# Performance work log

Hardware: AMD Instinct MI355X
Metric: run time of the kernel (lower is better)

Reference implementation:

```python
import jax, jax.numpy as jnp
import numpy as np

EMBED, HEADS, FF, WIN = 512, 8, 2048, 64
SIGMA, PSTRENGTH, PERIOD, THRESH = 2.0, 1.0, 100.0, 0.0


def layer_norm(x, g, b, eps=1e-5):
    mu = jnp.mean(x, axis=-1, keepdims=True)
    var = jnp.var(x, axis=-1, keepdims=True)
    return (x - mu) * jax.lax.rsqrt(var + eps) * g + b


def setup_inputs() -> dict:
    key = jax.random.key(0)
    ks = jax.random.split(key, 16)
    s = 1.0 / np.sqrt(EMBED)
    sf = 1.0 / np.sqrt(FF)
    inp = {
        "src": jax.random.normal(ks[0], (8, 2048, EMBED), dtype=jnp.float32),
        "Wq": jax.random.normal(ks[1], (EMBED, EMBED), dtype=jnp.float32) * s,
        "bq": jnp.zeros((EMBED,), jnp.float32),
        "Wk": jax.random.normal(ks[2], (EMBED, EMBED), dtype=jnp.float32) * s,
        "bk": jnp.zeros((EMBED,), jnp.float32),
        "Wv": jax.random.normal(ks[3], (EMBED, EMBED), dtype=jnp.float32) * s,
        "bv": jnp.zeros((EMBED,), jnp.float32),
        "Wo": jax.random.normal(ks[4], (EMBED, EMBED), dtype=jnp.float32) * s,
        "bo": jnp.zeros((EMBED,), jnp.float32),
        "Wg": jax.random.normal(ks[5], (EMBED, 1), dtype=jnp.float32) * s,
        "bg": jnp.zeros((1,), jnp.float32),
        "W1": jax.random.normal(ks[6], (EMBED, FF), dtype=jnp.float32) * s,
        "b1": jnp.zeros((FF,), jnp.float32),
        "W2": jax.random.normal(ks[7], (FF, EMBED), dtype=jnp.float32) * sf,
        "b2": jnp.zeros((EMBED,), jnp.float32),
        "ln1_g": jnp.ones((EMBED,), jnp.float32),
        "ln1_b": jnp.zeros((EMBED,), jnp.float32),
        "ln2_g": jnp.ones((EMBED,), jnp.float32),
        "ln2_b": jnp.zeros((EMBED,), jnp.float32),
    }
    return inp


def gated_sparse_attn(x, Wq, bq, Wk, bk, Wv, bv, Wo, bo, Wg, bg):
    B, S, D = x.shape
    H, dh = HEADS, D // HEADS
    q = (x @ Wq + bq).reshape(B, S, H, dh).transpose(0, 2, 1, 3)  # [B,H,S,dh]
    k = (x @ Wk + bk).reshape(B, S, H, dh).transpose(0, 2, 1, 3)
    v = (x @ Wv + bv).reshape(B, S, H, dh).transpose(0, 2, 1, 3)
    scores = jnp.einsum('bhqd,bhkd->bhqk', q, k) / jnp.sqrt(jnp.float32(dh))
    idx = jnp.arange(S, dtype=jnp.float32)
    dist = idx[:, None] - idx[None, :]  # [S,S]
    gauss_bias = jnp.exp(-(dist * dist) / (2.0 * SIGMA * SIGMA))
    per_bias = PSTRENGTH * jnp.cos(2.0 * jnp.pi * dist / PERIOD)
    scores = scores + gauss_bias + per_bias  # positional biases baked into scores
    local = jnp.abs(dist) <= WIN  # local-window sparsity mask
    scores = jnp.where(local, scores, jnp.float32(-1e9))
    attn = jax.nn.softmax(scores, axis=-1)
    out = jnp.einsum('bhqk,bhkd->bhqd', attn, v)
    out = out.transpose(0, 2, 1, 3).reshape(B, S, D) @ Wo + bo
    gate = jax.nn.sigmoid(x @ Wg + bg)  # [B,S,1] learned gating
    gate = jnp.where(gate > THRESH, gate, jnp.float32(0.0))
    return gate * out


def reference(src, Wq, bq, Wk, bk, Wv, bv, Wo, bo, Wg, bg, W1, b1, W2, b2, ln1_g, ln1_b, ln2_g, ln2_b):
    # dropout is identity in eval mode
    attn_out = gated_sparse_attn(src, Wq, bq, Wk, bk, Wv, bv, Wo, bo, Wg, bg)
    x = layer_norm(src + attn_out, ln1_g, ln1_b)
    ff = jax.nn.relu(x @ W1 + b1) @ W2 + b2
    return layer_norm(x + ff, ln2_g, ln2_b)
```

## Files before the change

kernel.cpp:

```cpp
#include <hip/hip_runtime.h>
#include <hip/hip_bf16.h>
#include <math.h>

#define S_LEN   2048
#define D_MOD   512
#define N_HEADS 8
#define D_HEAD  64
#define FF_DIM  2048
#define M_ROWS  16384
#define BHSD    8388608

typedef __attribute__((ext_vector_type(8))) __bf16 bf16x8;
typedef __attribute__((ext_vector_type(4))) float  f32x4;
typedef unsigned short u16;

__device__ __forceinline__ u16 f2bf(float f) {
  unsigned u = __float_as_uint(f);
  u += 0x7fffu + ((u >> 16) & 1u);
  return (u16)(u >> 16);
}
__device__ __forceinline__ float bf2f(u16 h) { return __uint_as_float(((unsigned)h) << 16); }

__device__ __forceinline__ f32x4 mfma16(bf16x8 a, bf16x8 b, f32x4 c) {
  return __builtin_amdgcn_mfma_f32_16x16x32_bf16(a, b, c, 0, 0, 0);
}

__device__ __forceinline__ void async16(void* lds, const void* g) {
  __builtin_amdgcn_global_load_lds(
      (const __attribute__((address_space(1))) unsigned int*)g,
      (__attribute__((address_space(3))) unsigned int*)lds, 16, 0, 0);
}

#define BAR()    asm volatile("s_barrier" ::: "memory")
#define WAITV(n) asm volatile("s_waitcnt vmcnt(" #n ")" ::: "memory")
#define WAITL()  asm volatile("s_waitcnt lgkmcnt(0)" ::: "memory")

__device__ __forceinline__ int swz384(int row, int bir) {
  return row * 384 + ((bir & ~127) | ((bir ^ ((row & 7) << 4)) & 127));
}

__global__ __launch_bounds__(256) void cvt_gate(const float* __restrict__ src,
                                                const float* __restrict__ Wg,
                                                const float* __restrict__ bg,
                                                u16* __restrict__ xb,
                                                float* __restrict__ gate) {
  const int wid = threadIdx.x >> 6, lane = threadIdx.x & 63;
  const size_t row = (size_t)blockIdx.x * 4 + wid;
  const float4* s = reinterpret_cast<const float4*>(src + row * D_MOD);
  const float4* w = reinterpret_cast<const float4*>(Wg);
  float4 a0 = s[lane * 2], a1 = s[lane * 2 + 1];
  float4 w0 = w[lane * 2], w1 = w[lane * 2 + 1];
  float acc = a0.x * w0.x + a0.y * w0.y + a0.z * w0.z + a0.w * w0.w +
              a1.x * w1.x + a1.y * w1.y + a1.z * w1.z + a1.w * w1.w;
#pragma unroll
  for (int m = 1; m < 64; m <<= 1) acc += __shfl_xor(acc, m);
  ushort4 h0, h1;
  h0.x = f2bf(a0.x); h0.y = f2bf(a0.y); h0.z = f2bf(a0.z); h0.w = f2bf(a0.w);
  h1.x = f2bf(a1.x); h1.y = f2bf(a1.y); h1.z = f2bf(a1.z); h1.w = f2bf(a1.w);
  ushort4* ob = reinterpret_cast<ushort4*>(xb + row * D_MOD);
  ob[lane * 2] = h0; ob[lane * 2 + 1] = h1;
  if (lane == 0) {
    float g = 1.f / (1.f + expf(-(acc + bg[0])));
    gate[row] = g > 0.f ? g : 0.f;
  }
}

__global__ void transpose_cvt(const float* __restrict__ in, u16* __restrict__ out,
                              int K, int N) {
  __shared__ float t[32][33];
  const int n0 = blockIdx.x * 32, k0 = blockIdx.y * 32;
  const int tx = threadIdx.x, ty = threadIdx.y;
#pragma unroll
  for (int i = 0; i < 4; ++i)
    t[ty + 8 * i][tx] = in[(size_t)(k0 + ty + 8 * i) * N + n0 + tx];
  __syncthreads();
#pragma unroll
  for (int i = 0; i < 4; ++i)
    out[(size_t)(n0 + ty + 8 * i) * K + k0 + tx] = f2bf(t[tx][ty + 8 * i]);
}

__global__ __launch_bounds__(256) void ln1_k(const float* __restrict__ in,
                                             const float* __restrict__ gam,
                                             const float* __restrict__ bet,
                                             u16* __restrict__ outb) {
  const int wid = threadIdx.x >> 6, lane = threadIdx.x & 63;
  const size_t row = (size_t)blockIdx.x * 4 + wid;
  const float4* p = reinterpret_cast<const float4*>(in + row * D_MOD);
  float4 v0 = p[lane * 2], v1 = p[lane * 2 + 1];
  float s  = v0.x + v0.y + v0.z + v0.w + v1.x + v1.y + v1.z + v1.w;
  float s2 = v0.x * v0.x + v0.y * v0.y + v0.z * v0.z + v0.w * v0.w +
             v1.x * v1.x + v1.y * v1.y + v1.z * v1.z + v1.w * v1.w;
#pragma unroll
  for (int m = 1; m < 64; m <<= 1) { s += __shfl_xor(s, m); s2 += __shfl_xor(s2, m); }
  const float mu = s * (1.0f / 512.0f);
  const float var = s2 * (1.0f / 512.0f) - mu * mu;
  const float rs = 1.0f / sqrtf(var + 1e-5f);
  const float4* gp = reinterpret_cast<const float4*>(gam);
  const float4* bp = reinterpret_cast<const float4*>(bet);
  float4 g0 = gp[lane * 2], g1 = gp[lane * 2 + 1];
  float4 b0 = bp[lane * 2], b1 = bp[lane * 2 + 1];
  ushort4 h0, h1;
  h0.x = f2bf((v0.x - mu) * rs * g0.x + b0.x);  h0.y = f2bf((v0.y - mu) * rs * g0.y + b0.y);
  h0.z = f2bf((v0.z - mu) * rs * g0.z + b0.z);  h0.w = f2bf((v0.w - mu) * rs * g0.w + b0.w);
  h1.x = f2bf((v1.x - mu) * rs * g1.x + b1.x);  h1.y = f2bf((v1.y - mu) * rs * g1.y + b1.y);
  h1.z = f2bf((v1.z - mu) * rs * g1.z + b1.z);  h1.w = f2bf((v1.w - mu) * rs * g1.w + b1.w);
  ushort4* ob = reinterpret_cast<ushort4*>(outb + row * D_MOD);
  ob[lane * 2] = h0; ob[lane * 2 + 1] = h1;
}

__global__ __launch_bounds__(256) void ln2red_k(const u16* __restrict__ xb,
                                                const float* __restrict__ p0,
                                                const float* __restrict__ p1,
                                                const float* __restrict__ b2,
                                                const float* __restrict__ gam,
                                                const float* __restrict__ bet,
                                                float* __restrict__ out) {
  const int wid = threadIdx.x >> 6, lane = threadIdx.x & 63;
  const size_t row = (size_t)blockIdx.x * 4 + wid;
  const size_t base = row * D_MOD;
  const ushort4* xp = reinterpret_cast<const ushort4*>(xb + base);
  const float4* q0 = reinterpret_cast<const float4*>(p0 + base);
  const float4* q1 = reinterpret_cast<const float4*>(p1 + base);
  const float4* bb = reinterpret_cast<const float4*>(b2);
  ushort4 h0 = xp[lane * 2], h1 = xp[lane * 2 + 1];
  float4 a0 = q0[lane * 2], a1 = q0[lane * 2 + 1];
  float4 c0 = q1[lane * 2], c1 = q1[lane * 2 + 1];
  float4 d0 = bb[lane * 2], d1 = bb[lane * 2 + 1];
  float4 v0, v1;
  v0.x = bf2f(h0.x) + a0.x + c0.x + d0.x;  v0.y = bf2f(h0.y) + a0.y + c0.y + d0.y;
  v0.z = bf2f(h0.z) + a0.z + c0.z + d0.z;  v0.w = bf2f(h0.w) + a0.w + c0.w + d0.w;
  v1.x = bf2f(h1.x) + a1.x + c1.x + d1.x;  v1.y = bf2f(h1.y) + a1.y + c1.y + d1.y;
  v1.z = bf2f(h1.z) + a1.z + c1.z + d1.z;  v1.w = bf2f(h1.w) + a1.w + c1.w + d1.w;
  float s  = v0.x + v0.y + v0.z + v0.w + v1.x + v1.y + v1.z + v1.w;
  float s2 = v0.x * v0.x + v0.y * v0.y + v0.z * v0.z + v0.w * v0.w +
             v1.x * v1.x + v1.y * v1.y + v1.z * v1.z + v1.w * v1.w;
#pragma unroll
  for (int m = 1; m < 64; m <<= 1) { s += __shfl_xor(s, m); s2 += __shfl_xor(s2, m); }
  const float mu = s * (1.0f / 512.0f);
  const float var = s2 * (1.0f / 512.0f) - mu * mu;
  const float rs = 1.0f / sqrtf(var + 1e-5f);
  const float4* gp = reinterpret_cast<const float4*>(gam);
  const float4* bp = reinterpret_cast<const float4*>(bet);
  float4 g0 = gp[lane * 2], g1 = gp[lane * 2 + 1];
  float4 e0 = bp[lane * 2], e1 = bp[lane * 2 + 1];
  float4 o0, o1;
  o0.x = (v0.x - mu) * rs * g0.x + e0.x;  o0.y = (v0.y - mu) * rs * g0.y + e0.y;
  o0.z = (v0.z - mu) * rs * g0.z + e0.z;  o0.w = (v0.w - mu) * rs * g0.w + e0.w;
  o1.x = (v1.x - mu) * rs * g1.x + e1.x;  o1.y = (v1.y - mu) * rs * g1.y + e1.y;
  o1.z = (v1.z - mu) * rs * g1.z + e1.z;  o1.w = (v1.w - mu) * rs * g1.w + e1.w;
  float4* q = reinterpret_cast<float4*>(out + base);
  q[lane * 2] = o0; q[lane * 2 + 1] = o1;
}

struct EpiArgs {
  const float* b0; const float* b1; const float* b2;
  const float* add; const float* gate;
  float* outf; float* outf2; u16* outb;
};

template<int EPI, int LD, int NT, int KSLICE, int GX, int GY>
__device__ __forceinline__ void gemm256_body(const u16* __restrict__ A,
                                             const u16* __restrict__ Bt, EpiArgs e) {
  extern __shared__ char smem[];
  char* Asb = smem;
  char* Bsb = smem + 65536;
  const int tid = threadIdx.x;
  const int wid = tid >> 6, lane = tid & 63;
  const int sub = lane >> 4, lc = lane & 15;
  const int wr = wid >> 2, wcn = wid & 3;

  const int nwg = (int)(gridDim.x * gridDim.y * gridDim.z);
  const int orig = ((int)blockIdx.z * (int)gridDim.y + (int)blockIdx.y) * (int)gridDim.x + (int)blockIdx.x;
  const int cpx = nwg >> 3;
  const int wg = (orig & 7) * cpx + (orig >> 3);
  const int bx = wg % GX;
  const int by = (wg / GX) % GY;
  const int bz = wg / (GX * GY);
  const int m0 = by * 256, n0 = bx * 256;
  const int kb = KSLICE * bz;

  const u16* Ab = A + (size_t)m0 * LD;
  const u16* Bb = Bt + (size_t)n0 * LD;

  f32x4 acc[8][4];
#pragma unroll
  for (int i = 0; i < 8; ++i)
#pragma unroll
    for (int j = 0; j < 4; ++j) acc[i][j] = (f32x4){0.f, 0.f, 0.f, 0.f};

  const int lr0 = tid >> 3;
  const int sl  = tid & 7;

#define STAGE(BASE, SRC, BUF, KT)                                              \
  {                                                                            \
    const int kk_ = kb + (KT) * 64;                                            \
    _Pragma("unroll")                                                          \
    for (int r_ = 0; r_ < 4; ++r_) {                                           \
      const int lr_ = r_ * 64 + lr0;                                           \
      async16((BASE) + (BUF) * 32768 + r_ * 8192 + wid * 1024,                 \
              (SRC) + (size_t)lr_ * LD + kk_ + ((sl ^ (lr_ & 7)) << 3));       \
    }                                                                          \
  }
#define LDFRAG(BASE, ROW, KS) \
  (*reinterpret_cast<const bf16x8*>((BASE) + (ROW) * 128 + ((((KS) * 64) + sub * 16) ^ (((ROW) & 7) << 4))))

  STAGE(Bsb, Bb, 0, 0);
  STAGE(Asb, Ab, 0, 0);
  STAGE(Bsb, Bb, 1, 1);
  STAGE(Asb, Ab, 1, 1);
  WAITV(8);
  BAR();

  for (int t = 0; t < NT; ++t) {
    const int buf = t & 1;
    char* Abl = Asb + buf * 32768;
    char* Bbl = Bsb + buf * 32768;
    bf16x8 af[4][2], bfr[2][2][2];
#pragma unroll
    for (int f = 0; f < 4; ++f) {
      const int row = wr * 128 + f * 16 + lc;
#pragma unroll
      for (int ks = 0; ks < 2; ++ks) af[f][ks] = LDFRAG(Abl, row, ks);
    }
#pragma unroll
    for (int f = 0; f < 2; ++f) {
      const int row = wcn * 64 + f * 16 + lc;
#pragma unroll
      for (int ks = 0; ks < 2; ++ks) bfr[0][f][ks] = LDFRAG(Bbl, row, ks);
    }
    __builtin_amdgcn_s_setprio(1);
#pragma unroll
    for (int f = 0; f < 4; ++f)
#pragma unroll
      for (int c = 0; c < 2; ++c)
#pragma unroll
        for (int ks = 0; ks < 2; ++ks)
          acc[f][c] = mfma16(af[f][ks], bfr[0][c][ks], acc[f][c]);
    __builtin_amdgcn_s_setprio(0);
    BAR();
#pragma unroll
    for (int f = 0; f < 2; ++f) {
      const int row = wcn * 64 + 32 + f * 16 + lc;
#pragma unroll
      for (int ks = 0; ks < 2; ++ks) bfr[1][f][ks] = LDFRAG(Bbl, row, ks);
    }
    __builtin_amdgcn_s_setprio(1);
#pragma unroll
    for (int f = 0; f < 4; ++f)
#pragma unroll
      for (int c = 0; c < 2; ++c)
#pragma unroll
        for (int ks = 0; ks < 2; ++ks)
          acc[f][2 + c] = mfma16(af[f][ks], bfr[1][c][ks], acc[f][2 + c]);
    __builtin_amdgcn_s_setprio(0);
    WAITL();
    BAR();
    if (t + 2 < NT) STAGE(Bsb, Bb, buf, t + 2);
#pragma unroll
    for (int f = 0; f < 4; ++f) {
      const int row = wr * 128 + 64 + f * 16 + lc;
#pragma unroll
      for (int ks = 0; ks < 2; ++ks) af[f][ks] = LDFRAG(Abl, row, ks);
    }
    __builtin_amdgcn_s_setprio(1);
#pragma unroll
    for (int f = 0; f < 4; ++f)
#pragma unroll
      for (int c = 0; c < 2; ++c)
#pragma unroll
        for (int ks = 0; ks < 2; ++ks)
          acc[4 + f][2 + c] = mfma16(af[f][ks], bfr[1][c][ks], acc[4 + f][2 + c]);
    __builtin_amdgcn_s_setprio(0);
    WAITL();
    BAR();
    if (t + 2 < NT) STAGE(Asb, Ab, buf, t + 2);
    __builtin_amdgcn_s_setprio(1);
#pragma unroll
    for (int f = 0; f < 4; ++f)
#pragma unroll
      for (int c = 0; c < 2; ++c)
#pragma unroll
        for (int ks = 0; ks < 2; ++ks)
          acc[4 + f][c] = mfma16(af[f][ks], bfr[0][c][ks], acc[4 + f][c]);
    __builtin_amdgcn_s_setprio(0);
    if (t + 1 < NT) {
      if (t + 2 < NT) { WAITV(8); } else { WAITV(0); }
      BAR();
    }
  }
#undef STAGE
#undef LDFRAG

#pragma unroll
  for (int fr = 0; fr < 8; ++fr) {
    const int row0 = m0 + wr * 128 + fr * 16 + sub * 4;
#pragma unroll
    for (int fc = 0; fc < 4; ++fc) {
      const int col = n0 + wcn * 64 + fc * 16 + lc;
      f32x4 v = acc[fr][fc];
#pragma unroll
      for (int i = 0; i < 4; ++i) {
        const int row = row0 + i;
        const float val = v[i];
        if constexpr (EPI == 0) {
          const int which = col >> 9, nn = col & 511;
          const int hh = nn >> 6, dd = nn & 63;
          const float* bp = (which == 0) ? e.b0 : (which == 1) ? e.b1 : e.b2;
          const int bb = row >> 11, ss = row & 2047;
          e.outb[(size_t)which * BHSD + (((size_t)bb * N_HEADS + hh) * S_LEN + ss) * D_HEAD + dd]
              = f2bf(val + bp[nn]);
        } else if constexpr (EPI == 2) {
          float o = val + e.b0[col];
          e.outb[(size_t)row * FF_DIM + col] = f2bf(o > 0.f ? o : 0.f);
        } else {
          float* dst = (bz == 0) ? e.outf : e.outf2;
          dst[(size_t)row * D_MOD + col] = val;
        }
      }
    }
  }
}

__global__ __launch_bounds__(512, 2) void k_qkv(const u16* __restrict__ A, const u16* __restrict__ B, EpiArgs e) {
  gemm256_body<0, 512, 8, 0, 6, 64>(A, B, e);
}
__global__ __launch_bounds__(512, 2) void k_ff1(const u16* __restrict__ A, const u16* __restrict__ B, EpiArgs e) {
  gemm256_body<2, 512, 8, 0, 8, 64>(A, B, e);
}
__global__ __launch_bounds__(512, 2) void k_ff2(const u16* __restrict__ A, const u16* __restrict__ B, EpiArgs e) {
  gemm256_body<4, 2048, 16, 1024, 2, 64>(A, B, e);
}

__global__ __launch_bounds__(256)
void k_proj(const u16* __restrict__ A, const u16* __restrict__ Bt,
            const float* __restrict__ bo, const float* __restrict__ add,
            const float* __restrict__ gate, float* __restrict__ outf) {
  __shared__ __align__(16) u16 As[128 * 64];
  __shared__ __align__(16) u16 Bs[128 * 64];
  const int tid = threadIdx.x;
  const int wid = tid >> 6, lane = tid & 63;
  const int wr = wid >> 1, wc = wid & 1;
  const int sub = lane >> 4, lc = lane & 15;
  const int K = 512;
  const int orig = (int)blockIdx.y * 4 + (int)blockIdx.x;
  const int wg = (orig & 7) * 64 + (orig >> 3);
  const int m0 = (wg >> 2) * 128, n0 = (wg & 3) * 128;

  f32x4 acc[4][4];
#pragma unroll
  for (int i = 0; i < 4; ++i)
#pragma unroll
    for (int j = 0; j < 4; ++j) acc[i][j] = (f32x4){0.f, 0.f, 0.f, 0.f};

  for (int k0 = 0; k0 < K; k0 += 64) {
#pragma unroll
    for (int i = 0; i < 4; ++i) {
      const int ldso = (wid * 4 + i) * 1024;
      const int o = ldso + lane * 16;
      const int r = o >> 7;
      const int c = (o & 127) >> 1;
      async16((char*)As + ldso, A  + (size_t)(m0 + r) * K + k0 + c);
      async16((char*)Bs + ldso, Bt + (size_t)(n0 + r) * K + k0 + c);
    }
    __syncthreads();
#pragma unroll
    for (int ks = 0; ks < 2; ++ks) {
      bf16x8 a[4], b[4];
#pragma unroll
      for (int i = 0; i < 4; ++i)
        a[i] = *reinterpret_cast<const bf16x8*>(&As[(wr * 64 + i * 16 + lc) * 64 + ks * 32 + sub * 8]);
#pragma unroll
      for (int j = 0; j < 4; ++j)
        b[j] = *reinterpret_cast<const bf16x8*>(&Bs[(wc * 64 + j * 16 + lc) * 64 + ks * 32 + sub * 8]);
#pragma unroll
      for (int i = 0; i < 4; ++i)
#pragma unroll
        for (int j = 0; j < 4; ++j) acc[i][j] = mfma16(a[i], b[j], acc[i][j]);
    }
    __syncthreads();
  }

#pragma unroll
  for (int i = 0; i < 4; ++i) {
    const int row0 = m0 + wr * 64 + i * 16 + sub * 4;
#pragma unroll
    for (int j = 0; j < 4; ++j) {
      const int col = n0 + wc * 64 + j * 16 + lc;
      f32x4 v = acc[i][j];
#pragma unroll
      for (int r = 0; r < 4; ++r) {
        const int row = row0 + r;
        outf[(size_t)row * D_MOD + col] =
            add[(size_t)row * D_MOD + col] + gate[row] * (v[r] + bo[col]);
      }
    }
  }
}

__global__ __launch_bounds__(256)
void attn_k(const u16* __restrict__ Q, const u16* __restrict__ Kt,
            const u16* __restrict__ V, u16* __restrict__ Oflat) {
  __shared__ __align__(16) u16 VT[64 * 192];
  __shared__ __align__(16) u16 P [64 * 192];
  __shared__ float tab[256];
  const int tid = threadIdx.x;
  const int wid = tid >> 6, lane = tid & 63;
  const int sub = lane >> 4, lc = lane & 15;
  const int qb = blockIdx.x, bh = blockIdx.y;
  const int bb = bh >> 3, hh = bh & 7;
  const int q0 = qb * 64, kstart = q0 - 64;
  const u16* Qb = Q  + (size_t)bh * S_LEN * D_HEAD;
  const u16* Kb = Kt + (size_t)bh * S_LEN * D_HEAD;
  const u16* Vb = V  + (size_t)bh * S_LEN * D_HEAD;

  if (tid < 255) {
    const int di = tid - 127;
    const float fd = (float)di;
    tab[tid] = (di >= -64 && di <= 64)
        ? expf(-fd * fd * 0.125f) + cosf(0.06283185307179586f * fd)
        : -1e9f;
  }

#pragma unroll
  for (int i = 0; i < 6; ++i) {
    const int c = tid + 256 * i;
    const int kk = c >> 3, dc = (c & 7) * 8;
    const int kg = kstart + kk;
    uint4 val = {0u, 0u, 0u, 0u};
    if (kg >= 0 && kg < S_LEN)
      val = *reinterpret_cast<const uint4*>(Vb + (size_t)kg * D_HEAD + dc);
    const u16* pv = reinterpret_cast<const u16*>(&val);
#pragma unroll
    for (int j = 0; j < 8; ++j)
      *reinterpret_cast<u16*>(reinterpret_cast<char*>(VT) + swz384(dc + j, kk * 2)) = pv[j];
  }

  bf16x8 qf[2];
#pragma unroll
  for (int ks = 0; ks < 2; ++ks)
    qf[ks] = *reinterpret_cast<const bf16x8*>(Qb + (size_t)(q0 + wid * 16 + lc) * D_HEAD + ks * 32 + sub * 8);

  f32x4 sc[12];
#pragma unroll
  for (int t = 0; t < 12; ++t) sc[t] = (f32x4){0.f, 0.f, 0.f, 0.f};
#pragma unroll
  for (int ks = 0; ks < 2; ++ks)
#pragma unroll
    for (int t = 0; t < 12; ++t) {
      int kg = kstart + t * 16 + lc;
      int kc = kg < 0 ? 0 : (kg > S_LEN - 1 ? S_LEN - 1 : kg);
      bf16x8 kf = *reinterpret_cast<const bf16x8*>(Kb + (size_t)kc * D_HEAD + ks * 32 + sub * 8);
      sc[t] = mfma16(qf[ks], kf, sc[t]);
    }
  __syncthreads();

  float rmax[4] = {-3e38f, -3e38f, -3e38f, -3e38f};
#pragma unroll
  for (int t = 0; t < 12; ++t) {
    const int kk = t * 16 + lc;
    const int kg = kstart + kk;
    const bool valid = (kg >= 0) && (kg < S_LEN);
#pragma unroll
    for (int r = 0; r < 4; ++r) {
      const int qrow = wid * 16 + sub * 4 + r;
      const float bias = valid ? tab[qrow - kk + 191] : -1e9f;
      const float sv = sc[t][r] * 0.125f + bias;
      sc[t][r] = sv;
      rmax[r] = fmaxf(rmax[r], sv);
    }
  }
#pragma unroll
  for (int m = 1; m < 16; m <<= 1)
#pragma unroll
    for (int r = 0; r < 4; ++r) rmax[r] = fmaxf(rmax[r], __shfl_xor(rmax[r], m));
  float rsum[4] = {0.f, 0.f, 0.f, 0.f};
#pragma unroll
  for (int t = 0; t < 12; ++t)
#pragma unroll
    for (int r = 0; r < 4; ++r) {
      const float p = expf(sc[t][r] - rmax[r]);
      sc[t][r] = p; rsum[r] += p;
    }
#pragma unroll
  for (int m = 1; m < 16; m <<= 1)
#pragma unroll
    for (int r = 0; r < 4; ++r) rsum[r] += __shfl_xor(rsum[r], m);
  float rinv[4];
#pragma unroll
  for (int r = 0; r < 4; ++r) rinv[r] = 1.0f / rsum[r];
#pragma unroll
  for (int t = 0; t < 12; ++t)
#pragma unroll
    for (int r = 0; r < 4; ++r) {
      const int qrow = wid * 16 + sub * 4 + r;
      *reinterpret_cast<u16*>(reinterpret_cast<char*>(P) + swz384(qrow, (t * 16 + lc) * 2))
          = f2bf(sc[t][r] * rinv[r]);
    }
  __syncthreads();

  f32x4 oacc[4];
#pragma unroll
  for (int t = 0; t < 4; ++t) oacc[t] = (f32x4){0.f, 0.f, 0.f, 0.f};
  const int arow = wid * 16 + lc;
#pragma unroll
  for (int ks = 0; ks < 6; ++ks) {
    const int bir = ks * 64 + sub * 16;
    bf16x8 pa = *reinterpret_cast<const bf16x8*>(reinterpret_cast<char*>(P) + swz384(arow, bir));
#pragma unroll
    for (int t = 0; t < 4; ++t) {
      bf16x8 vb = *reinterpret_cast<const bf16x8*>(reinterpret_cast<char*>(VT) + swz384(t * 16 + lc, bir));
      oacc[t] = mfma16(pa, vb, oacc[t]);
    }
  }

  const size_t obase = ((size_t)bb * S_LEN + q0) * D_MOD + hh * D_HEAD;
#pragma unroll
  for (int t = 0; t < 4; ++t)
#pragma unroll
    for (int r = 0; r < 4; ++r) {
      const int qrow = wid * 16 + sub * 4 + r;
      Oflat[obase + (size_t)qrow * D_MOD + t * 16 + lc] = f2bf(oacc[t][r]);
    }
}

extern "C" void kernel_launch(void* const* d_in, const int* in_sizes, int n_in,
                              void* d_out, int out_size, void* d_ws, size_t ws_size,
                              hipStream_t stream) {
  (void)in_sizes; (void)n_in; (void)out_size; (void)ws_size;
  const float* src  = (const float*)d_in[0];
  const float* Wq   = (const float*)d_in[1];
  const float* bq   = (const float*)d_in[2];
  const float* Wk   = (const float*)d_in[3];
  const float* bk   = (const float*)d_in[4];
  const float* Wv   = (const float*)d_in[5];
  const float* bv   = (const float*)d_in[6];
  const float* Wo   = (const float*)d_in[7];
  const float* bo   = (const float*)d_in[8];
  const float* Wg   = (const float*)d_in[9];
  const float* bg   = (const float*)d_in[10];
  const float* W1   = (const float*)d_in[11];
  const float* b1   = (const float*)d_in[12];
  const float* W2   = (const float*)d_in[13];
  const float* b2   = (const float*)d_in[14];
  const float* ln1g = (const float*)d_in[15];
  const float* ln1b = (const float*)d_in[16];
  const float* ln2g = (const float*)d_in[17];
  const float* ln2b = (const float*)d_in[18];
  float* out = (float*)d_out;

  char* ws = (char*)d_ws;
  u16*   WqkvT  = (u16*)  (ws + 0);
  u16*   WoT    = (u16*)  (ws + 1572864);
  u16*   W1T    = (u16*)  (ws + 2097152);
  u16*   W2T    = (u16*)  (ws + 4194304);
  float* gatef  = (float*)(ws + 6291456);
  u16*   Xbf    = (u16*)  (ws + 6356992);
  u16*   QKVbf  = (u16*)  (ws + 23134208);
  u16*   attnfl = (u16*)  (ws + 73465856);
  float* y1     = (float*)(ws + 90243072);
  u16*   xbf2   = (u16*)  (ws + 123797504);
  u16*   hbuf   = Xbf;
  float* p0     = y1;
  float* p1     = (float*)(ws + 140574720);

  (void)hipFuncSetAttribute((const void*)k_qkv, hipFuncAttributeMaxDynamicSharedMemorySize, 131072);
  (void)hipFuncSetAttribute((const void*)k_ff1, hipFuncAttributeMaxDynamicSharedMemorySize, 131072);
  (void)hipFuncSetAttribute((const void*)k_ff2, hipFuncAttributeMaxDynamicSharedMemorySize, 131072);

  dim3 tb(32, 8);
  cvt_gate<<<4096, 256, 0, stream>>>(src, Wg, bg, Xbf, gatef);
  transpose_cvt<<<dim3(16, 16), tb, 0, stream>>>(Wq, WqkvT,             512, 512);
  transpose_cvt<<<dim3(16, 16), tb, 0, stream>>>(Wk, WqkvT + 512 * 512, 512, 512);
  transpose_cvt<<<dim3(16, 16), tb, 0, stream>>>(Wv, WqkvT + 2 * 512 * 512, 512, 512);
  transpose_cvt<<<dim3(16, 16), tb, 0, stream>>>(Wo, WoT, 512, 512);
  transpose_cvt<<<dim3(64, 16), tb, 0, stream>>>(W1, W1T, 512, 2048);
  transpose_cvt<<<dim3(16, 64), tb, 0, stream>>>(W2, W2T, 2048, 512);

  EpiArgs e1{bq, bk, bv, nullptr, nullptr, nullptr, nullptr, QKVbf};
  k_qkv<<<dim3(6, 64, 1), 512, 131072, stream>>>(Xbf, WqkvT, e1);

  attn_k<<<dim3(32, 64), 256, 0, stream>>>(QKVbf, QKVbf + BHSD, QKVbf + 2 * BHSD, attnfl);

  k_proj<<<dim3(4, 128), 256, 0, stream>>>(attnfl, WoT, bo, src, gatef, y1);

  ln1_k<<<4096, 256, 0, stream>>>(y1, ln1g, ln1b, xbf2);

  EpiArgs e3{b1, nullptr, nullptr, nullptr, nullptr, nullptr, nullptr, hbuf};
  k_ff1<<<dim3(8, 64, 1), 512, 131072, stream>>>(xbf2, W1T, e3);

  EpiArgs e4{nullptr, nullptr, nullptr, nullptr, nullptr, p0, p1, nullptr};
  k_ff2<<<dim3(2, 64, 2), 512, 131072, stream>>>(hbuf, W2T, e4);

  ln2red_k<<<4096, 256, 0, stream>>>(xbf2, p0, p1, b2, ln2g, ln2b, out);
}
```

Before: 235.0 us.

## Route output projection through shared 256-tile GEMM with split-K bf16 partials

Replaces the dedicated 128x128 output-projection kernel with the shared 256-tile LDS GEMM body, using split-K over two z-slices that write bf16 partials. The gating, bias and residual add move into a new fused LN1 kernel that sums the two partials. FF2 partials are also stored in bf16 instead of fp32 to halve that traffic. Fast-math __expf/__cosf intrinsics replace expf/cosf in the attention and gate paths, at some cost in partial-sum precision.

```diff
diff --git a/kernel.cpp b/kernel.cpp
--- a/kernel.cpp
+++ b/kernel.cpp
@@ -60,7 +60,7 @@
   ushort4* ob = reinterpret_cast<ushort4*>(xb + row * D_MOD);
   ob[lane * 2] = h0; ob[lane * 2 + 1] = h1;
   if (lane == 0) {
-    float g = 1.f / (1.f + expf(-(acc + bg[0])));
+    float g = 1.f / (1.f + __expf(-(acc + bg[0])));
     gate[row] = g > 0.f ? g : 0.f;
   }
 }
@@ -79,14 +79,35 @@
     out[(size_t)(n0 + ty + 8 * i) * K + k0 + tx] = f2bf(t[tx][ty + 8 * i]);
 }
 
-__global__ __launch_bounds__(256) void ln1_k(const float* __restrict__ in,
-                                             const float* __restrict__ gam,
-                                             const float* __restrict__ bet,
-                                             u16* __restrict__ outb) {
+__global__ __launch_bounds__(256) void ln1red_k(const float* __restrict__ src,
+                                                const float* __restrict__ gate,
+                                                const u16* __restrict__ p0,
+                                                const u16* __restrict__ p1,
+                                                const float* __restrict__ bo,
+                                                const float* __restrict__ gam,
+                                                const float* __restrict__ bet,
+                                                u16* __restrict__ outb) {
   const int wid = threadIdx.x >> 6, lane = threadIdx.x & 63;
   const size_t row = (size_t)blockIdx.x * 4 + wid;
-  const float4* p = reinterpret_cast<const float4*>(in + row * D_MOD);
-  float4 v0 = p[lane * 2], v1 = p[lane * 2 + 1];
+  const size_t base = row * D_MOD;
+  const float g = gate[row];
+  const float4*  sp = reinterpret_cast<const float4*>(src + base);
+  const ushort4* a  = reinterpret_cast<const ushort4*>(p0 + base);
+  const ushort4* c  = reinterpret_cast<const ushort4*>(p1 + base);
+  const float4*  bb = reinterpret_cast<const float4*>(bo);
+  float4 s0 = sp[lane * 2], s1 = sp[lane * 2 + 1];
+  ushort4 a0 = a[lane * 2], a1 = a[lane * 2 + 1];
+  ushort4 c0 = c[lane * 2], c1 = c[lane * 2 + 1];
+  float4 d0 = bb[lane * 2], d1 = bb[lane * 2 + 1];
+  float4 v0, v1;
+  v0.x = s0.x + g * (bf2f(a0.x) + bf2f(c0.x) + d0.x);
+  v0.y = s0.y + g * (bf2f(a0.y) + bf2f(c0.y) + d0.y);
+  v0.z = s0.z + g * (bf2f(a0.z) + bf2f(c0.z) + d0.z);
+  v0.w = s0.w + g * (bf2f(a0.w) + bf2f(c0.w) + d0.w);
+  v1.x = s1.x + g * (bf2f(a1.x) + bf2f(c1.x) + d1.x);
+  v1.y = s1.y + g * (bf2f(a1.y) + bf2f(c1.y) + d1.y);
+  v1.z = s1.z + g * (bf2f(a1.z) + bf2f(c1.z) + d1.z);
+  v1.w = s1.w + g * (bf2f(a1.w) + bf2f(c1.w) + d1.w);
   float s  = v0.x + v0.y + v0.z + v0.w + v1.x + v1.y + v1.z + v1.w;
   float s2 = v0.x * v0.x + v0.y * v0.y + v0.z * v0.z + v0.w * v0.w +
              v1.x * v1.x + v1.y * v1.y + v1.z * v1.z + v1.w * v1.w;
@@ -98,19 +119,19 @@
   const float4* gp = reinterpret_cast<const float4*>(gam);
   const float4* bp = reinterpret_cast<const float4*>(bet);
   float4 g0 = gp[lane * 2], g1 = gp[lane * 2 + 1];
-  float4 b0 = bp[lane * 2], b1 = bp[lane * 2 + 1];
+  float4 e0 = bp[lane * 2], e1 = bp[lane * 2 + 1];
   ushort4 h0, h1;
-  h0.x = f2bf((v0.x - mu) * rs * g0.x + b0.x);  h0.y = f2bf((v0.y - mu) * rs * g0.y + b0.y);
-  h0.z = f2bf((v0.z - mu) * rs * g0.z + b0.z);  h0.w = f2bf((v0.w - mu) * rs * g0.w + b0.w);
-  h1.x = f2bf((v1.x - mu) * rs * g1.x + b1.x);  h1.y = f2bf((v1.y - mu) * rs * g1.y + b1.y);
-  h1.z = f2bf((v1.z - mu) * rs * g1.z + b1.z);  h1.w = f2bf((v1.w - mu) * rs * g1.w + b1.w);
-  ushort4* ob = reinterpret_cast<ushort4*>(outb + row * D_MOD);
+  h0.x = f2bf((v0.x - mu) * rs * g0.x + e0.x);  h0.y = f2bf((v0.y - mu) * rs * g0.y + e0.y);
+  h0.z = f2bf((v0.z - mu) * rs * g0.z + e0.z);  h0.w = f2bf((v0.w - mu) * rs * g0.w + e0.w);
+  h1.x = f2bf((v1.x - mu) * rs * g1.x + e1.x);  h1.y = f2bf((v1.y - mu) * rs * g1.y + e1.y);
+  h1.z = f2bf((v1.z - mu) * rs * g1.z + e1.z);  h1.w = f2bf((v1.w - mu) * rs * g1.w + e1.w);
+  ushort4* ob = reinterpret_cast<ushort4*>(outb + base);
   ob[lane * 2] = h0; ob[lane * 2 + 1] = h1;
 }
 
 __global__ __launch_bounds__(256) void ln2red_k(const u16* __restrict__ xb,
-                                                const float* __restrict__ p0,
-                                                const float* __restrict__ p1,
+                                                const u16* __restrict__ p0,
+                                                const u16* __restrict__ p1,
                                                 const float* __restrict__ b2,
                                                 const float* __restrict__ gam,
                                                 const float* __restrict__ bet,
@@ -119,18 +140,22 @@
   const size_t row = (size_t)blockIdx.x * 4 + wid;
   const size_t base = row * D_MOD;
   const ushort4* xp = reinterpret_cast<const ushort4*>(xb + base);
-  const float4* q0 = reinterpret_cast<const float4*>(p0 + base);
-  const float4* q1 = reinterpret_cast<const float4*>(p1 + base);
+  const ushort4* q0 = reinterpret_cast<const ushort4*>(p0 + base);
+  const ushort4* q1 = reinterpret_cast<const ushort4*>(p1 + base);
   const float4* bb = reinterpret_cast<const float4*>(b2);
   ushort4 h0 = xp[lane * 2], h1 = xp[lane * 2 + 1];
-  float4 a0 = q0[lane * 2], a1 = q0[lane * 2 + 1];
-  float4 c0 = q1[lane * 2], c1 = q1[lane * 2 + 1];
+  ushort4 a0 = q0[lane * 2], a1 = q0[lane * 2 + 1];
+  ushort4 c0 = q1[lane * 2], c1 = q1[lane * 2 + 1];
   float4 d0 = bb[lane * 2], d1 = bb[lane * 2 + 1];
   float4 v0, v1;
-  v0.x = bf2f(h0.x) + a0.x + c0.x + d0.x;  v0.y = bf2f(h0.y) + a0.y + c0.y + d0.y;
-  v0.z = bf2f(h0.z) + a0.z + c0.z + d0.z;  v0.w = bf2f(h0.w) + a0.w + c0.w + d0.w;
-  v1.x = bf2f(h1.x) + a1.x + c1.x + d1.x;  v1.y = bf2f(h1.y) + a1.y + c1.y + d1.y;
-  v1.z = bf2f(h1.z) + a1.z + c1.z + d1.z;  v1.w = bf2f(h1.w) + a1.w + c1.w + d1.w;
+  v0.x = bf2f(h0.x) + bf2f(a0.x) + bf2f(c0.x) + d0.x;
+  v0.y = bf2f(h0.y) + bf2f(a0.y) + bf2f(c0.y) + d0.y;
+  v0.z = bf2f(h0.z) + bf2f(a0.z) + bf2f(c0.z) + d0.z;
+  v0.w = bf2f(h0.w) + bf2f(a0.w) + bf2f(c0.w) + d0.w;
+  v1.x = bf2f(h1.x) + bf2f(a1.x) + bf2f(c1.x) + d1.x;
+  v1.y = bf2f(h1.y) + bf2f(a1.y) + bf2f(c1.y) + d1.y;
+  v1.z = bf2f(h1.z) + bf2f(a1.z) + bf2f(c1.z) + d1.z;
+  v1.w = bf2f(h1.w) + bf2f(a1.w) + bf2f(c1.w) + d1.w;
   float s  = v0.x + v0.y + v0.z + v0.w + v1.x + v1.y + v1.z + v1.w;
   float s2 = v0.x * v0.x + v0.y * v0.y + v0.z * v0.z + v0.w * v0.w +
              v1.x * v1.x + v1.y * v1.y + v1.z * v1.z + v1.w * v1.w;
@@ -154,8 +179,7 @@
 
 struct EpiArgs {
   const float* b0; const float* b1; const float* b2;
-  const float* add; const float* gate;
-  float* outf; float* outf2; u16* outb;
+  float* outf; u16* outb; u16* outb2;
 };
 
 template<int EPI, int LD, int NT, int KSLICE, int GX, int GY>
@@ -313,8 +337,8 @@
           float o = val + e.b0[col];
           e.outb[(size_t)row * FF_DIM + col] = f2bf(o > 0.f ? o : 0.f);
         } else {
-          float* dst = (bz == 0) ? e.outf : e.outf2;
-          dst[(size_t)row * D_MOD + col] = val;
+          u16* dst = (bz == 0) ? e.outb : e.outb2;
+          dst[(size_t)row * D_MOD + col] = f2bf(val);
         }
       }
     }
@@ -330,71 +354,8 @@
 __global__ __launch_bounds__(512, 2) void k_ff2(const u16* __restrict__ A, const u16* __restrict__ B, EpiArgs e) {
   gemm256_body<4, 2048, 16, 1024, 2, 64>(A, B, e);
 }
-
-__global__ __launch_bounds__(256)
-void k_proj(const u16* __restrict__ A, const u16* __restrict__ Bt,
-            const float* __restrict__ bo, const float* __restrict__ add,
-            const float* __restrict__ gate, float* __restrict__ outf) {
-  __shared__ __align__(16) u16 As[128 * 64];
-  __shared__ __align__(16) u16 Bs[128 * 64];
-  const int tid = threadIdx.x;
-  const int wid = tid >> 6, lane = tid & 63;
-  const int wr = wid >> 1, wc = wid & 1;
-  const int sub = lane >> 4, lc = lane & 15;
-  const int K = 512;
-  const int orig = (int)blockIdx.y * 4 + (int)blockIdx.x;
-  const int wg = (orig & 7) * 64 + (orig >> 3);
-  const int m0 = (wg >> 2) * 128, n0 = (wg & 3) * 128;
-
-  f32x4 acc[4][4];
-#pragma unroll
-  for (int i = 0; i < 4; ++i)
-#pragma unroll
-    for (int j = 0; j < 4; ++j) acc[i][j] = (f32x4){0.f, 0.f, 0.f, 0.f};
-
-  for (int k0 = 0; k0 < K; k0 += 64) {
-#pragma unroll
-    for (int i = 0; i < 4; ++i) {
-      const int ldso = (wid * 4 + i) * 1024;
-      const int o = ldso + lane * 16;
-      const int r = o >> 7;
-      const int c = (o & 127) >> 1;
-      async16((char*)As + ldso, A  + (size_t)(m0 + r) * K + k0 + c);
-      async16((char*)Bs + ldso, Bt + (size_t)(n0 + r) * K + k0 + c);
-    }
-    __syncthreads();
-#pragma unroll
-    for (int ks = 0; ks < 2; ++ks) {
-      bf16x8 a[4], b[4];
-#pragma unroll
-      for (int i = 0; i < 4; ++i)
-        a[i] = *reinterpret_cast<const bf16x8*>(&As[(wr * 64 + i * 16 + lc) * 64 + ks * 32 + sub * 8]);
-#pragma unroll
-      for (int j = 0; j < 4; ++j)
-        b[j] = *reinterpret_cast<const bf16x8*>(&Bs[(wc * 64 + j * 16 + lc) * 64 + ks * 32 + sub * 8]);
-#pragma unroll
-      for (int i = 0; i < 4; ++i)
-#pragma unroll
-        for (int j = 0; j < 4; ++j) acc[i][j] = mfma16(a[i], b[j], acc[i][j]);
-    }
-    __syncthreads();
-  }
-
-#pragma unroll
-  for (int i = 0; i < 4; ++i) {
-    const int row0 = m0 + wr * 64 + i * 16 + sub * 4;
-#pragma unroll
-    for (int j = 0; j < 4; ++j) {
-      const int col = n0 + wc * 64 + j * 16 + lc;
-      f32x4 v = acc[i][j];
-#pragma unroll
-      for (int r = 0; r < 4; ++r) {
-        const int row = row0 + r;
-        outf[(size_t)row * D_MOD + col] =
-            add[(size_t)row * D_MOD + col] + gate[row] * (v[r] + bo[col]);
-      }
-    }
-  }
+__global__ __launch_bounds__(512, 2) void k_proj(const u16* __restrict__ A, const u16* __restrict__ B, EpiArgs e) {
+  gemm256_body<4, 512, 4, 256, 2, 64>(A, B, e);
 }
 
 __global__ __launch_bounds__(256)
@@ -417,7 +378,7 @@
     const int di = tid - 127;
     const float fd = (float)di;
     tab[tid] = (di >= -64 && di <= 64)
-        ? expf(-fd * fd * 0.125f) + cosf(0.06283185307179586f * fd)
+        ? __expf(-fd * fd * 0.125f) + __cosf(0.06283185307179586f * fd)
         : -1e9f;
   }
 
@@ -478,7 +439,7 @@
   for (int t = 0; t < 12; ++t)
 #pragma unroll
     for (int r = 0; r < 4; ++r) {
-      const float p = expf(sc[t][r] - rmax[r]);
+      const float p = __expf(sc[t][r] - rmax[r]);
       sc[t][r] = p; rsum[r] += p;
     }
 #pragma unroll
@@ -557,15 +518,17 @@
   u16*   Xbf    = (u16*)  (ws + 6356992);
   u16*   QKVbf  = (u16*)  (ws + 23134208);
   u16*   attnfl = (u16*)  (ws + 73465856);
-  float* y1     = (float*)(ws + 90243072);
+  u16*   pr0    = (u16*)  (ws + 90243072);
+  u16*   pr1    = (u16*)  (ws + 107020288);
   u16*   xbf2   = (u16*)  (ws + 123797504);
   u16*   hbuf   = Xbf;
-  float* p0     = y1;
-  float* p1     = (float*)(ws + 140574720);
-
-  (void)hipFuncSetAttribute((const void*)k_qkv, hipFuncAttributeMaxDynamicSharedMemorySize, 131072);
-  (void)hipFuncSetAttribute((const void*)k_ff1, hipFuncAttributeMaxDynamicSharedMemorySize, 131072);
-  (void)hipFuncSetAttribute((const void*)k_ff2, hipFuncAttributeMaxDynamicSharedMemorySize, 131072);
+  u16*   pf0    = pr0;
+  u16*   pf1    = pr1;
+
+  (void)hipFuncSetAttribute((const void*)k_qkv,  hipFuncAttributeMaxDynamicSharedMemorySize, 131072);
+  (void)hipFuncSetAttribute((const void*)k_ff1,  hipFuncAttributeMaxDynamicSharedMemorySize, 131072);
+  (void)hipFuncSetAttribute((const void*)k_ff2,  hipFuncAttributeMaxDynamicSharedMemorySize, 131072);
+  (void)hipFuncSetAttribute((const void*)k_proj, hipFuncAttributeMaxDynamicSharedMemorySize, 131072);
 
   dim3 tb(32, 8);
   cvt_gate<<<4096, 256, 0, stream>>>(src, Wg, bg, Xbf, gatef);
@@ -576,20 +539,21 @@
   transpose_cvt<<<dim3(64, 16), tb, 0, stream>>>(W1, W1T, 512, 2048);
   transpose_cvt<<<dim3(16, 64), tb, 0, stream>>>(W2, W2T, 2048, 512);
 
-  EpiArgs e1{bq, bk, bv, nullptr, nullptr, nullptr, nullptr, QKVbf};
+  EpiArgs e1{bq, bk, bv, nullptr, QKVbf, nullptr};
   k_qkv<<<dim3(6, 64, 1), 512, 131072, stream>>>(Xbf, WqkvT, e1);
 
   attn_k<<<dim3(32, 64), 256, 0, stream>>>(QKVbf, QKVbf + BHSD, QKVbf + 2 * BHSD, attnfl);
 
-  k_proj<<<dim3(4, 128), 256, 0, stream>>>(attnfl, WoT, bo, src, gatef, y1);
-
-  ln1_k<<<4096, 256, 0, stream>>>(y1, ln1g, ln1b, xbf2);
-
-  EpiArgs e3{b1, nullptr, nullptr, nullptr, nullptr, nullptr, nullptr, hbuf};
+  EpiArgs e2{nullptr, nullptr, nullptr, nullptr, pr0, pr1};
+  k_proj<<<dim3(2, 64, 2), 512, 131072, stream>>>(attnfl, WoT, e2);
+
+  ln1red_k<<<4096, 256, 0, stream>>>(src, gatef, pr0, pr1, bo, ln1g, ln1b, xbf2);
+
+  EpiArgs e3{b1, nullptr, nullptr, nullptr, hbuf, nullptr};
   k_ff1<<<dim3(8, 64, 1), 512, 131072, stream>>>(xbf2, W1T, e3);
 
-  EpiArgs e4{nullptr, nullptr, nullptr, nullptr, nullptr, p0, p1, nullptr};
+  EpiArgs e4{nullptr, nullptr, nullptr, nullptr, pf0, pf1};
   k_ff2<<<dim3(2, 64, 2), 512, 131072, stream>>>(hbuf, W2T, e4);
 
-  ln2red_k<<<4096, 256, 0, stream>>>(xbf2, p0, p1, b2, ln2g, ln2b, out);
-}
+  ln2red_k<<<4096, 256, 0, stream>>>(xbf2, pf0, pf1, b2, ln2g, ln2b, out);
+}
```

After: 222.6 us. 5.3% less time.
